# Optimization experiments

Measured on AMD Instinct MI355X. Metric: run time of the kernel, lower is better.

## Reference

```python
import jax, jax.numpy as jnp
import numpy as np

B, P, D, K = 16384, 20, 128, 5  # batch, nodes per sample, embed dim, knn k


def setup_inputs() -> dict:
    key = jax.random.key(0)
    ks = jax.random.split(key, 11)
    def rn(k, shape, scale=0.05):
        return jax.random.normal(k, shape, dtype=jnp.float32) * scale
    return {
        "x": jax.random.normal(ks[0], (B, P, D), dtype=jnp.float32),
        "W1": rn(ks[1], (300, D)), "b1": rn(ks[2], (300,)),
        "W2": rn(ks[3], (100, 300)), "b2": rn(ks[4], (100,)),
        "W3": rn(ks[5], (50, 100)), "b3": rn(ks[6], (50,)),
        "W4": rn(ks[7], (100, P * 50)), "b4": rn(ks[8], (100,)),
        "W5": rn(ks[9], (3, 100)), "b5": rn(ks[10], (3,)),
    }


def _gcn_agg_matrix(x, k):
    """Build the 20x20 GCN aggregation matrix equivalent to PyG GCNConv over the
    concatenated per-sample kNN edge lists (node ids shared 0..P-1 across batch)."""
    b, p, d = x.shape
    sq = jnp.sum(x * x, axis=-1)                                  # (B,P)
    d2 = sq[:, :, None] + sq[:, None, :] - 2.0 * jnp.einsum('bpd,bqd->bpq', x, x)
    d2 = jax.lax.stop_gradient(d2)  # indices only; squared dist preserves ordering
    _, idx = jax.lax.top_k(-d2, k + 1)                            # smallest k+1, sorted
    nbr = idx[..., 1:]                                            # (B,P,k) drop self
    src = jnp.broadcast_to(jnp.arange(p)[None, :, None], nbr.shape)
    flat = (nbr * p + src).reshape(-1)                            # C[v,u] multiplicity
    C = jnp.zeros((p * p,), jnp.float32).at[flat].add(1.0).reshape(p, p)
    deg = C.sum(axis=1) + 1.0                                     # in-degree + self-loop
    dinv = 1.0 / jnp.sqrt(deg)
    return dinv[:, None] * C * dinv[None, :] + jnp.diag(dinv * dinv)


def reference(x, W1, b1, W2, b2, W3, b3, W4, b4, W5, b5):
    h = x
    for W, b in ((W1, b1), (W2, b2), (W3, b3)):
        M = _gcn_agg_matrix(h, K)                                 # (P,P)
        h = jax.nn.relu(jnp.einsum('vu,bud->bvd', M, h @ W.T) + b)
    h = h.reshape(h.shape[0], -1)                                 # (B, P*50)
    h = jax.nn.relu(h @ W4.T + b4)
    logits = h @ W5.T + b5
    return jax.nn.softmax(logits, axis=1)
```

## Files before the change

kernel.cpp:

```cpp
#include <hip/hip_runtime.h>
#include <math.h>

#define BB 16384
#define P 20
#define NT 512

typedef short v8s __attribute__((ext_vector_type(8)));
typedef _Float16 v8h __attribute__((ext_vector_type(8)));
typedef float f32x4 __attribute__((ext_vector_type(4)));
typedef float f32x16 __attribute__((ext_vector_type(16)));

#define NELEM ((size_t)BB * P * 320)
__device__ unsigned int g_C[3][P * P];
__device__ __align__(16) unsigned short g_bufA[NELEM + 4096];
__device__ __align__(16) unsigned short g_bufB[NELEM + 4096];
__device__ __align__(16) unsigned short g_W1b[320 * 128];
__device__ __align__(16) unsigned short g_W2b[128 * 320];
__device__ __align__(16) unsigned short g_W3b[64 * 128];
__device__ __align__(16) unsigned short g_W4b[112 * 1024];
__device__ __align__(16) float g_b1p[320];
__device__ __align__(16) float g_b2p[128];
__device__ __align__(16) float g_b3p[64];
__device__ __align__(16) float g_b4p[112];

__device__ inline float bf2f(unsigned short u) {
    union { unsigned int i; float f; } c; c.i = ((unsigned int)u) << 16; return c.f;
}
__device__ inline unsigned short f2bf(float f) {
    union { float f; unsigned int i; } c; c.f = f;
    unsigned int u = c.i + 0x7fffu + ((c.i >> 16) & 1u);
    return (unsigned short)(u >> 16);
}

__global__ void zero_C_kernel() { g_C[blockIdx.x][threadIdx.x] = 0u; }

__global__ void prep_kernel(const float* __restrict__ W1, const float* __restrict__ b1,
                            const float* __restrict__ W2, const float* __restrict__ b2,
                            const float* __restrict__ W3, const float* __restrict__ b3,
                            const float* __restrict__ W4, const float* __restrict__ b4) {
    const int stride = gridDim.x * blockDim.x;
    const int id = blockIdx.x * blockDim.x + threadIdx.x;
    for (int i = id; i < 320 * 128; i += stride) { int n = i >> 7, k = i & 127;
        g_W1b[i] = (n < 300) ? f2bf(W1[n * 128 + k]) : 0; }
    for (int i = id; i < 128 * 320; i += stride) { int n = i / 320, k = i - n * 320;
        g_W2b[i] = (n < 100 && k < 300) ? f2bf(W2[n * 300 + k]) : 0; }
    for (int i = id; i < 64 * 128; i += stride) { int n = i >> 7, k = i & 127;
        g_W3b[i] = (n < 50 && k < 100) ? f2bf(W3[n * 100 + k]) : 0; }
    for (int i = id; i < 112 * 1024; i += stride) { int n = i >> 10, k = i & 1023;
        g_W4b[i] = (n < 100 && k < 1000) ? f2bf(W4[n * 1000 + k]) : 0; }
    for (int i = id; i < 320; i += stride) g_b1p[i] = (i < 300) ? b1[i] : 0.f;
    for (int i = id; i < 128; i += stride) g_b2p[i] = (i < 100) ? b2[i] : 0.f;
    for (int i = id; i < 64;  i += stride) g_b3p[i] = (i < 50)  ? b3[i] : 0.f;
    for (int i = id; i < 112; i += stride) g_b4p[i] = (i < 100) ? b4[i] : 0.f;
}

__global__ __launch_bounds__(NT)
void knn1_mfma_kernel(const float* __restrict__ x) {
    __shared__ float Gs[8][P * 21];
    __shared__ unsigned int hist[P * P];
    const int t = threadIdx.x, w = t >> 6, lane = t & 63;
    const int m31 = lane & 31, half = lane >> 5;
    const int mrow = (m31 < P) ? m31 : (P - 1);
    for (int i = t; i < P * P; i += NT) hist[i] = 0;
    for (int pass = 0; pass < 2; ++pass) {
        const size_t s = (size_t)blockIdx.x * 16 + pass * 8 + w;
        const float* rp = x + s * (size_t)(P * 128) + (size_t)mrow * 128 + half * 8;
        f32x16 acc;
#pragma unroll
        for (int i = 0; i < 16; ++i) acc[i] = 0.f;
#pragma unroll
        for (int ks = 0; ks < 8; ++ks) {
            float4 f0 = *(const float4*)(rp + ks * 16);
            float4 f1 = *(const float4*)(rp + ks * 16 + 4);
            float fv[8] = {f0.x, f0.y, f0.z, f0.w, f1.x, f1.y, f1.z, f1.w};
            v8h hi, lo;
#pragma unroll
            for (int j = 0; j < 8; ++j) {
                _Float16 hv = (_Float16)fv[j];
                hi[j] = hv;
                lo[j] = (_Float16)(fv[j] - (float)hv);
            }
            acc = __builtin_amdgcn_mfma_f32_32x32x16_f16(hi, hi, acc, 0, 0, 0);
            acc = __builtin_amdgcn_mfma_f32_32x32x16_f16(hi, lo, acc, 0, 0, 0);
            acc = __builtin_amdgcn_mfma_f32_32x32x16_f16(lo, hi, acc, 0, 0, 0);
            acc = __builtin_amdgcn_mfma_f32_32x32x16_f16(lo, lo, acc, 0, 0, 0);
        }
        float* G = &Gs[w][0];
        if (m31 < P) {
#pragma unroll
            for (int r = 0; r < 16; ++r) {
                int row = (r & 3) + 8 * (r >> 2) + 4 * half;
                if (row < P) G[row * 21 + m31] = acc[r];
            }
        }
        __syncthreads();
        if (lane < P) {
            const int p = lane;
            float d2[P];
            const float gpp = G[p * 21 + p];
#pragma unroll
            for (int u = 0; u < P; ++u)
                d2[u] = (u == p) ? 0.f : gpp + G[u * 21 + u] - 2.f * G[p * 21 + u];
            float pv = -3.0e38f; int pi = -1;
            for (int it = 0; it < 6; ++it) {
                float best = 3.0e38f; int bq = 0;
#pragma unroll
                for (int u = 0; u < P; ++u) {
                    float vu = d2[u];
                    bool cand = (vu > pv) || (vu == pv && u > pi);
                    if (cand && vu < best) { best = vu; bq = u; }
                }
                if (it > 0) atomicAdd(&hist[bq * P + p], 1u);
                pv = best; pi = bq;
            }
        }
        __syncthreads();
    }
    if (t < P * P && hist[t]) atomicAdd(&g_C[0][t], hist[t]);
}

template<int D, int CIDX>
__global__ __launch_bounds__(NT)
void knn_mfma_kernel() {
    __shared__ float Gs[8][P * 21];
    __shared__ unsigned int hist[P * P];
    const int t = threadIdx.x, w = t >> 6, lane = t & 63;
    const int m31 = lane & 31, half = lane >> 5;
    for (int i = t; i < P * P; i += NT) hist[i] = 0;
    for (int pass = 0; pass < 2; ++pass) {
        const size_t s = (size_t)blockIdx.x * 16 + pass * 8 + w;
        const unsigned short* rp = g_bufB + s * (P * D) + (size_t)m31 * D + half * 8;
        f32x16 acc;
#pragma unroll
        for (int i = 0; i < 16; ++i) acc[i] = 0.f;
        for (int ks = 0; ks < D / 16; ++ks) {
            v8s z = *(const v8s*)(rp + ks * 16);
            acc = __builtin_amdgcn_mfma_f32_32x32x16_bf16(z, z, acc, 0, 0, 0);
        }
        float* G = &Gs[w][0];
        if (m31 < P) {
#pragma unroll
            for (int r = 0; r < 16; ++r) {
                int row = (r & 3) + 8 * (r >> 2) + 4 * half;
                if (row < P) G[row * 21 + m31] = acc[r];
            }
        }
        __syncthreads();
        if (lane < P) {
            const int p = lane;
            float d2[P];
            const float gpp = G[p * 21 + p];
#pragma unroll
            for (int u = 0; u < P; ++u)
                d2[u] = (u == p) ? 0.f : gpp + G[u * 21 + u] - 2.f * G[p * 21 + u];
            float pv = -3.0e38f; int pi = -1;
            for (int it = 0; it < 6; ++it) {
                float best = 3.0e38f; int bq = 0;
#pragma unroll
                for (int u = 0; u < P; ++u) {
                    float vu = d2[u];
                    bool cand = (vu > pv) || (vu == pv && u > pi);
                    if (cand && vu < best) { best = vu; bq = u; }
                }
                if (it > 0) atomicAdd(&hist[bq * P + p], 1u);
                pv = best; pi = bq;
            }
        }
        __syncthreads();
    }
    if (t < P * P && hist[t]) atomicAdd(&g_C[CIDX][t], hist[t]);
}

__device__ inline void compute_M_512(const unsigned int* __restrict__ Cg,
                                     float* Ms, float* dinv, int t) {
    for (int i = t; i < P * P; i += 512) Ms[i] = (float)Cg[i];
    __syncthreads();
    if (t < P) {
        float deg = 1.f;
        for (int u = 0; u < P; ++u) deg += Ms[t * P + u];
        dinv[t] = 1.f / sqrtf(deg);
    }
    __syncthreads();
    for (int i = t; i < P * P; i += 512) {
        int v = i / P, u = i - v * P;
        float m = dinv[v] * Ms[i] * dinv[u];
        if (v == u) m += dinv[v] * dinv[v];
        Ms[i] = m;
    }
    __syncthreads();
}

template<int D, int CIDX>
__global__ __launch_bounds__(512)
void agg_mfma_kernel(const float* __restrict__ xin) {
    constexpr int NCB = D / 32;
    __shared__ float Ms[P * P];
    __shared__ float dinv[P];
    const int t = threadIdx.x, w = t >> 6, lane = t & 63;
    const int n31 = lane & 31, half = lane >> 5;
    compute_M_512(g_C[CIDX], Ms, dinv, t);
    v8s mhi[2], mlo[2];
#pragma unroll
    for (int kc = 0; kc < 2; ++kc)
#pragma unroll
        for (int j = 0; j < 8; ++j) {
            const int u = kc * 16 + half * 8 + j;
            const int v = n31;
            const float m = (v < P && u < P) ? Ms[v * P + u] : 0.f;
            const unsigned short h16 = f2bf(m);
            mhi[kc][j] = (short)h16;
            mlo[kc][j] = (short)f2bf(m - bf2f(h16));
        }
    const size_t s = (size_t)blockIdx.x * 8 + w;
    unsigned short* zout = g_bufA + s * (size_t)(P * D);
    const float* xr = xin + s * (size_t)(P * D);
#pragma unroll
    for (int cb = 0; cb < NCB; ++cb) {
        v8s bh0, bl0, bh1, bl1;
#pragma unroll
        for (int j = 0; j < 8; ++j) {
            const int u0 = half * 8 + j;
            int u1 = 16 + half * 8 + j; if (u1 > P - 1) u1 = P - 1;
            const float x0 = xr[(size_t)u0 * D + cb * 32 + n31];
            const float x1 = xr[(size_t)u1 * D + cb * 32 + n31];
            const unsigned short h0 = f2bf(x0), h1 = f2bf(x1);
            bh0[j] = (short)h0; bl0[j] = (short)f2bf(x0 - bf2f(h0));
            bh1[j] = (short)h1; bl1[j] = (short)f2bf(x1 - bf2f(h1));
        }
        f32x16 acc;
#pragma unroll
        for (int i = 0; i < 16; ++i) acc[i] = 0.f;
        acc = __builtin_amdgcn_mfma_f32_32x32x16_bf16(mhi[0], bh0, acc, 0, 0, 0);
        acc = __builtin_amdgcn_mfma_f32_32x32x16_bf16(mhi[0], bl0, acc, 0, 0, 0);
        acc = __builtin_amdgcn_mfma_f32_32x32x16_bf16(mlo[0], bh0, acc, 0, 0, 0);
        acc = __builtin_amdgcn_mfma_f32_32x32x16_bf16(mlo[0], bl0, acc, 0, 0, 0);
        acc = __builtin_amdgcn_mfma_f32_32x32x16_bf16(mhi[1], bh1, acc, 0, 0, 0);
        acc = __builtin_amdgcn_mfma_f32_32x32x16_bf16(mhi[1], bl1, acc, 0, 0, 0);
        acc = __builtin_amdgcn_mfma_f32_32x32x16_bf16(mlo[1], bh1, acc, 0, 0, 0);
        acc = __builtin_amdgcn_mfma_f32_32x32x16_bf16(mlo[1], bl1, acc, 0, 0, 0);
#pragma unroll
        for (int r = 0; r < 16; ++r) {
            const int row = (r & 3) + 8 * (r >> 2) + 4 * half;
            if (row < P)
                zout[(size_t)row * D + cb * 32 + n31] = f2bf(acc[r]);
        }
    }
}

template<int D, int CIDX, bool FLATOUT>
__global__ __launch_bounds__(512)
void agg_out_kernel() {
    constexpr int NCB = D / 32;
    __shared__ float Ms[P * P];
    __shared__ float dinv[P];
    const int t = threadIdx.x, w = t >> 6, lane = t & 63;
    const int n31 = lane & 31, half = lane >> 5;
    const float* __restrict__ bp = (CIDX == 1) ? g_b2p : g_b3p;
    compute_M_512(g_C[CIDX], Ms, dinv, t);
    v8s mhi[2], mlo[2];
#pragma unroll
    for (int kc = 0; kc < 2; ++kc)
#pragma unroll
        for (int j = 0; j < 8; ++j) {
            const int u = kc * 16 + half * 8 + j;
            const int v = n31;
            const float m = (v < P && u < P) ? Ms[v * P + u] : 0.f;
            const unsigned short h16 = f2bf(m);
            mhi[kc][j] = (short)h16;
            mlo[kc][j] = (short)f2bf(m - bf2f(h16));
        }
    const size_t s = (size_t)blockIdx.x * 8 + w;
    const unsigned short* yr = g_bufA + s * (size_t)(P * D);
#pragma unroll
    for (int cb = 0; cb < NCB; ++cb) {
        v8s b0, b1;
#pragma unroll
        for (int j = 0; j < 8; ++j) {
            const int u0 = half * 8 + j;
            int u1 = 16 + half * 8 + j; if (u1 > P - 1) u1 = P - 1;
            b0[j] = (short)yr[(size_t)u0 * D + cb * 32 + n31];
            b1[j] = (short)yr[(size_t)u1 * D + cb * 32 + n31];
        }
        f32x16 acc;
#pragma unroll
        for (int i = 0; i < 16; ++i) acc[i] = 0.f;
        acc = __builtin_amdgcn_mfma_f32_32x32x16_bf16(mhi[0], b0, acc, 0, 0, 0);
        acc = __builtin_amdgcn_mfma_f32_32x32x16_bf16(mlo[0], b0, acc, 0, 0, 0);
        acc = __builtin_amdgcn_mfma_f32_32x32x16_bf16(mhi[1], b1, acc, 0, 0, 0);
        acc = __builtin_amdgcn_mfma_f32_32x32x16_bf16(mlo[1], b1, acc, 0, 0, 0);
        const float bv = bp[cb * 32 + n31];
#pragma unroll
        for (int r = 0; r < 16; ++r) {
            const int row = (r & 3) + 8 * (r >> 2) + 4 * half;
            if (row < P) {
                const float val = fmaxf(acc[r] + bv, 0.f);
                if (FLATOUT) {
                    const int d = cb * 32 + n31;
                    if (d < 50)
                        g_bufB[s * 1024 + (size_t)row * 50 + d] = f2bf(val);
                } else {
                    g_bufB[(s * (size_t)P + row) * D + cb * 32 + n31] = f2bf(val);
                }
            }
        }
    }
}

__global__ __launch_bounds__(256)
void gemm2_kernel() {
    constexpr int KL = 72;
    __shared__ __align__(16) unsigned short As[128 * KL];
    __shared__ __align__(16) unsigned short Wsh[128 * KL];
    const int t = threadIdx.x, w = t >> 6, lane = t & 63;
    const int m15 = lane & 15, q = lane >> 4;
    const long row0 = (long)blockIdx.x * 128;
    f32x4 acc[2][8];
#pragma unroll
    for (int zr = 0; zr < 2; ++zr)
#pragma unroll
        for (int nf = 0; nf < 8; ++nf) acc[zr][nf] = 0.f;
    for (int kc = 0; kc < 5; ++kc) {
        __syncthreads();
        for (int i = t; i < 1024; i += 256) {
            const int r = i >> 3, c8 = i & 7;
            *(v8s*)&As[r * KL + c8 * 8] =
                *(const v8s*)(g_bufB + (size_t)(row0 + r) * 320 + kc * 64 + c8 * 8);
            *(v8s*)&Wsh[r * KL + c8 * 8] =
                *(const v8s*)(g_W2b + (size_t)r * 320 + kc * 64 + c8 * 8);
        }
        __syncthreads();
#pragma unroll
        for (int ks = 0; ks < 2; ++ks) {
            v8s af[2];
#pragma unroll
            for (int zr = 0; zr < 2; ++zr)
                af[zr] = *(const v8s*)&As[(w * 32 + zr * 16 + m15) * KL + ks * 32 + q * 8];
#pragma unroll
            for (int nf = 0; nf < 8; ++nf) {
                v8s wf = *(const v8s*)&Wsh[(nf * 16 + m15) * KL + ks * 32 + q * 8];
#pragma unroll
                for (int zr = 0; zr < 2; ++zr)
                    acc[zr][nf] = __builtin_amdgcn_mfma_f32_16x16x32_bf16(
                        wf, af[zr], acc[zr][nf], 0, 0, 0);
            }
        }
    }
#pragma unroll
    for (int zr = 0; zr < 2; ++zr) {
        const long m = row0 + w * 32 + zr * 16 + m15;
#pragma unroll
        for (int nf = 0; nf < 8; ++nf) {
            f32x4 c = acc[zr][nf];
            ushort4 o; o.x = f2bf(c[0]); o.y = f2bf(c[1]);
            o.z = f2bf(c[2]); o.w = f2bf(c[3]);
            *(ushort4*)(g_bufA + (size_t)m * 128 + nf * 16 + q * 4) = o;
        }
    }
}

template<int Kp, int Np, int ZR, bool FLAT, int WSEL, bool ATOB, int NSPLIT,
         int KSC, int NTHR, long MROWS, bool RAWBF16>
__global__ __launch_bounds__(NTHR)
void gemm_kernel() {
    constexpr int BN = Np / NSPLIT;
    constexpr int NF = BN / 16;
    constexpr int KS = Kp / 32;
    constexpr int CPT = KS / KSC;
    constexpr int KL = Kp + 8;
    constexpr int NW = NTHR / 64;
    constexpr int TM = NW * ZR * 16;
    constexpr long NTILE = MROWS / TM;
    static_assert(KS % KSC == 0, "KSC must divide KS");
    __shared__ __align__(16) unsigned short Ws[BN * KL];
    __shared__ __align__(16) float bs[BN];
    const unsigned short* __restrict__ Wb =
        (WSEL == 1) ? g_W1b : (WSEL == 2) ? g_W2b : (WSEL == 3) ? g_W3b : g_W4b;
    const float* __restrict__ bp =
        (WSEL == 1) ? g_b1p : (WSEL == 2) ? g_b2p : (WSEL == 3) ? g_b3p : g_b4p;
    const unsigned short* __restrict__ A = ATOB ? g_bufA : g_bufB;
    unsigned short* __restrict__ Hout = ATOB ? g_bufB : g_bufA;
    const int t = threadIdx.x, w = t >> 6, lane = t & 63;
    const int m15 = lane & 15, q = lane >> 4;
    const int n0 = blockIdx.y * BN;
    for (int i = t; i < BN * (Kp / 8); i += NTHR) {
        int r = i / (Kp / 8), c = i - r * (Kp / 8);
        *(v8s*)(&Ws[r * KL + c * 8]) = *(const v8s*)(Wb + (size_t)(n0 + r) * Kp + c * 8);
    }
    for (int i = t; i < BN; i += NTHR) bs[i] = bp[n0 + i];
    __syncthreads();

    v8s aC[ZR][KSC], aN[ZR][KSC];
    long tile = (long)blockIdx.x;
    if (tile < NTILE) {
        const unsigned short* ab =
            A + (size_t)(tile * TM + w * (ZR * 16) + m15) * Kp + q * 8;
#pragma unroll
        for (int zr = 0; zr < ZR; ++zr)
#pragma unroll
            for (int ks = 0; ks < KSC; ++ks)
                aC[zr][ks] = *(const v8s*)(ab + (size_t)zr * 16 * Kp + ks * 32);
    }
    for (; tile < NTILE; tile += gridDim.x) {
        f32x4 acc[ZR][NF];
#pragma unroll
        for (int zr = 0; zr < ZR; ++zr)
#pragma unroll
            for (int nf = 0; nf < NF; ++nf) acc[zr][nf] = 0.f;
        for (int c = 0; c < CPT; ++c) {
            const long ntile = (c + 1 < CPT) ? tile : tile + (long)gridDim.x;
            const int nk0 = (c + 1 < CPT) ? (c + 1) * KSC : 0;
            const bool hasNext = (ntile < NTILE);
            if (hasNext) {
                const unsigned short* ab =
                    A + (size_t)(ntile * TM + w * (ZR * 16) + m15) * Kp + nk0 * 32 + q * 8;
#pragma unroll
                for (int zr = 0; zr < ZR; ++zr)
#pragma unroll
                    for (int ks = 0; ks < KSC; ++ks)
                        aN[zr][ks] = *(const v8s*)(ab + (size_t)zr * 16 * Kp + ks * 32);
            }
#pragma unroll
            for (int nf = 0; nf < NF; ++nf) {
                v8s wr[KSC];
#pragma unroll
                for (int ks = 0; ks < KSC; ++ks)
                    wr[ks] = *(const v8s*)(&Ws[(nf * 16 + m15) * KL + (c * KSC + ks) * 32 + q * 8]);
#pragma unroll
                for (int ks = 0; ks < KSC; ++ks)
#pragma unroll
                    for (int zr = 0; zr < ZR; ++zr)
                        acc[zr][nf] = __builtin_amdgcn_mfma_f32_16x16x32_bf16(
                            wr[ks], aC[zr][ks], acc[zr][nf], 0, 0, 0);
            }
            if (hasNext) {
#pragma unroll
                for (int zr = 0; zr < ZR; ++zr)
#pragma unroll
                    for (int ks = 0; ks < KSC; ++ks) aC[zr][ks] = aN[zr][ks];
            }
        }
#pragma unroll
        for (int zr = 0; zr < ZR; ++zr) {
            const long m = tile * TM + w * (ZR * 16) + zr * 16 + m15;
#pragma unroll
            for (int nf = 0; nf < NF; ++nf) {
                f32x4 cc = acc[zr][nf];
                if (RAWBF16) {
                    ushort4 o; o.x = f2bf(cc[0]); o.y = f2bf(cc[1]);
                    o.z = f2bf(cc[2]); o.w = f2bf(cc[3]);
                    *(ushort4*)(Hout + (size_t)m * Np + n0 + nf * 16 + q * 4) = o;
                } else {
                    f32x4 b4 = *(const f32x4*)(&bs[nf * 16 + q * 4]);
                    float v0 = fmaxf(cc[0] + b4[0], 0.f), v1 = fmaxf(cc[1] + b4[1], 0.f);
                    float v2 = fmaxf(cc[2] + b4[2], 0.f), v3 = fmaxf(cc[3] + b4[3], 0.f);
                    if (!FLAT) {
                        ushort4 o; o.x = f2bf(v0); o.y = f2bf(v1); o.z = f2bf(v2); o.w = f2bf(v3);
                        *(ushort4*)(Hout + (size_t)m * Np + n0 + nf * 16 + q * 4) = o;
                    } else {
                        const int n0f = nf * 16 + q * 4;
                        if (n0f <= 48) {
                            const long s = m / 20; const int u = (int)(m - s * 20);
                            unsigned short* base = Hout + (size_t)s * 1024 + u * 50 + n0f;
                            unsigned int lo = (unsigned int)f2bf(v0) | ((unsigned int)f2bf(v1) << 16);
                            *(unsigned int*)(base) = lo;
                            if (n0f < 48) {
                                unsigned int hi = (unsigned int)f2bf(v2) | ((unsigned int)f2bf(v3) << 16);
                                *(unsigned int*)(base + 2) = hi;
                            }
                        }
                    }
                }
            }
        }
    }
}

__global__ __launch_bounds__(256)
void head_kernel(const float* __restrict__ W5, const float* __restrict__ b5,
                 float* __restrict__ out) {
    __shared__ float w5s[300];
    __shared__ float b5s[3];
    const int t = threadIdx.x;
    for (int i = t; i < 300; i += 256) w5s[i] = W5[i];
    if (t < 3) b5s[t] = b5[t];
    __syncthreads();
    const int s = blockIdx.x * 256 + t;
    const unsigned short* h = g_bufA + (size_t)s * 112;
    float a0 = b5s[0], a1 = b5s[1], a2 = b5s[2];
    for (int k = 0; k < 100; ++k) {
        float hv = bf2f(h[k]);
        a0 += hv * w5s[k]; a1 += hv * w5s[100 + k]; a2 += hv * w5s[200 + k];
    }
    float m = fmaxf(a0, fmaxf(a1, a2));
    float e0 = expf(a0 - m), e1 = expf(a1 - m), e2 = expf(a2 - m);
    float inv = 1.f / (e0 + e1 + e2);
    out[(size_t)s * 3 + 0] = e0 * inv;
    out[(size_t)s * 3 + 1] = e1 * inv;
    out[(size_t)s * 3 + 2] = e2 * inv;
}

extern "C" void kernel_launch(void* const* d_in, const int* in_sizes, int n_in,
                              void* d_out, int out_size, void* d_ws, size_t ws_size,
                              hipStream_t stream) {
    const float* x  = (const float*)d_in[0];
    const float* W1 = (const float*)d_in[1];
    const float* b1 = (const float*)d_in[2];
    const float* W2 = (const float*)d_in[3];
    const float* b2 = (const float*)d_in[4];
    const float* W3 = (const float*)d_in[5];
    const float* b3 = (const float*)d_in[6];
    const float* W4 = (const float*)d_in[7];
    const float* b4 = (const float*)d_in[8];
    const float* W5 = (const float*)d_in[9];
    const float* b5 = (const float*)d_in[10];
    float* out = (float*)d_out;

    zero_C_kernel<<<3, P * P, 0, stream>>>();
    prep_kernel<<<256, 256, 0, stream>>>(W1, b1, W2, b2, W3, b3, W4, b4);

    knn1_mfma_kernel<<<BB / 16, NT, 0, stream>>>(x);
    agg_mfma_kernel<128, 0><<<BB / 8, 512, 0, stream>>>(x);
    gemm_kernel<128, 320, 1, false, 1, true, 2, 4, 512, 327680L, false>
        <<<dim3(512, 2), 512, 0, stream>>>();

    knn_mfma_kernel<320, 1><<<BB / 16, NT, 0, stream>>>();
    gemm2_kernel<<<2560, 256, 0, stream>>>();
    agg_out_kernel<128, 1, false><<<BB / 8, 512, 0, stream>>>();

    knn_mfma_kernel<128, 2><<<BB / 16, NT, 0, stream>>>();
    gemm_kernel<128, 64, 2, false, 3, false, 1, 4, 256, 327680L, true>
        <<<dim3(512, 1), 256, 0, stream>>>();
    agg_out_kernel<64, 2, true><<<BB / 8, 512, 0, stream>>>();

    gemm_kernel<1024, 112, 1, false, 4, false, 7, 8, 256, 16384L, false>
        <<<dim3(256, 7), 256, 0, stream>>>();
    head_kernel<<<BB / 256, 256, 0, stream>>>(W5, b5, out);
}
```

Measured before the change: 808.1 us.

## Fuse layer-2 kNN graph build into the W2 GEMM kernel

```diff
diff --git a/kernel.cpp b/kernel.cpp
--- a/kernel.cpp
+++ b/kernel.cpp
@@ -32,14 +32,13 @@
     return (unsigned short)(u >> 16);
 }
 
-__global__ void zero_C_kernel() { g_C[blockIdx.x][threadIdx.x] = 0u; }
-
 __global__ void prep_kernel(const float* __restrict__ W1, const float* __restrict__ b1,
                             const float* __restrict__ W2, const float* __restrict__ b2,
                             const float* __restrict__ W3, const float* __restrict__ b3,
                             const float* __restrict__ W4, const float* __restrict__ b4) {
     const int stride = gridDim.x * blockDim.x;
     const int id = blockIdx.x * blockDim.x + threadIdx.x;
+    for (int i = id; i < 3 * P * P; i += stride) g_C[i / (P * P)][i % (P * P)] = 0u;
     for (int i = id; i < 320 * 128; i += stride) { int n = i >> 7, k = i & 127;
         g_W1b[i] = (n < 300) ? f2bf(W1[n * 128 + k]) : 0; }
     for (int i = id; i < 128 * 320; i += stride) { int n = i / 320, k = i - n * 320;
@@ -306,55 +305,93 @@
     }
 }
 
-__global__ __launch_bounds__(256)
-void gemm2_kernel() {
-    constexpr int KL = 72;
-    __shared__ __align__(16) unsigned short As[128 * KL];
-    __shared__ __align__(16) unsigned short Wsh[128 * KL];
+__global__ __launch_bounds__(640)
+void gemm2_knn_kernel() {
+    __shared__ __align__(16) unsigned short As[160 * 72];
+    __shared__ __align__(16) unsigned short Wsh[128 * 72];
+    __shared__ float Gs[8][P * 21];
+    __shared__ unsigned int hist[P * P];
     const int t = threadIdx.x, w = t >> 6, lane = t & 63;
+    const int m31 = lane & 31, half = lane >> 5;
     const int m15 = lane & 15, q = lane >> 4;
-    const long row0 = (long)blockIdx.x * 128;
-    f32x4 acc[2][8];
-#pragma unroll
-    for (int zr = 0; zr < 2; ++zr)
-#pragma unroll
-        for (int nf = 0; nf < 8; ++nf) acc[zr][nf] = 0.f;
+    const long row0 = (long)blockIdx.x * 160;
+    for (int i = t; i < P * P; i += 640) hist[i] = 0;
+    __syncthreads();
+    if (w < 8) {
+        const size_t s = (size_t)blockIdx.x * 8 + w;
+        const unsigned short* rp = g_bufB + s * (P * 320) + (size_t)m31 * 320 + half * 8;
+        f32x16 acc;
+#pragma unroll
+        for (int i = 0; i < 16; ++i) acc[i] = 0.f;
+        for (int ks = 0; ks < 20; ++ks) {
+            v8s z = *(const v8s*)(rp + ks * 16);
+            acc = __builtin_amdgcn_mfma_f32_32x32x16_bf16(z, z, acc, 0, 0, 0);
+        }
+        float* G = &Gs[w][0];
+        if (m31 < P) {
+#pragma unroll
+            for (int r = 0; r < 16; ++r) {
+                int row = (r & 3) + 8 * (r >> 2) + 4 * half;
+                if (row < P) G[row * 21 + m31] = acc[r];
+            }
+        }
+        if (lane < P) {
+            const int p = lane;
+            float d2[P];
+            const float gpp = G[p * 21 + p];
+#pragma unroll
+            for (int u = 0; u < P; ++u)
+                d2[u] = (u == p) ? 0.f : gpp + G[u * 21 + u] - 2.f * G[p * 21 + u];
+            float pv = -3.0e38f; int pi = -1;
+            for (int it = 0; it < 6; ++it) {
+                float best = 3.0e38f; int bq = 0;
+#pragma unroll
+                for (int u = 0; u < P; ++u) {
+                    float vu = d2[u];
+                    bool cand = (vu > pv) || (vu == pv && u > pi);
+                    if (cand && vu < best) { best = vu; bq = u; }
+                }
+                if (it > 0) atomicAdd(&hist[bq * P + p], 1u);
+                pv = best; pi = bq;
+            }
+        }
+    }
+    __syncthreads();
+    if (t < P * P && hist[t]) atomicAdd(&g_C[1][t], hist[t]);
+    f32x4 acc[8];
+#pragma unroll
+    for (int nf = 0; nf < 8; ++nf) acc[nf] = 0.f;
     for (int kc = 0; kc < 5; ++kc) {
         __syncthreads();
-        for (int i = t; i < 1024; i += 256) {
+        for (int i = t; i < 1280; i += 640) {
             const int r = i >> 3, c8 = i & 7;
-            *(v8s*)&As[r * KL + c8 * 8] =
+            *(v8s*)&As[r * 72 + c8 * 8] =
                 *(const v8s*)(g_bufB + (size_t)(row0 + r) * 320 + kc * 64 + c8 * 8);
-            *(v8s*)&Wsh[r * KL + c8 * 8] =
+        }
+        for (int i = t; i < 1024; i += 640) {
+            const int r = i >> 3, c8 = i & 7;
+            *(v8s*)&Wsh[r * 72 + c8 * 8] =
                 *(const v8s*)(g_W2b + (size_t)r * 320 + kc * 64 + c8 * 8);
         }
         __syncthreads();
 #pragma unroll
         for (int ks = 0; ks < 2; ++ks) {
-            v8s af[2];
-#pragma unroll
-            for (int zr = 0; zr < 2; ++zr)
-                af[zr] = *(const v8s*)&As[(w * 32 + zr * 16 + m15) * KL + ks * 32 + q * 8];
+            v8s af = *(const v8s*)&As[(w * 16 + m15) * 72 + ks * 32 + q * 8];
 #pragma unroll
             for (int nf = 0; nf < 8; ++nf) {
-                v8s wf = *(const v8s*)&Wsh[(nf * 16 + m15) * KL + ks * 32 + q * 8];
-#pragma unroll
-                for (int zr = 0; zr < 2; ++zr)
-                    acc[zr][nf] = __builtin_amdgcn_mfma_f32_16x16x32_bf16(
-                        wf, af[zr], acc[zr][nf], 0, 0, 0);
-            }
-        }
-    }
-#pragma unroll
-    for (int zr = 0; zr < 2; ++zr) {
-        const long m = row0 + w * 32 + zr * 16 + m15;
-#pragma unroll
-        for (int nf = 0; nf < 8; ++nf) {
-            f32x4 c = acc[zr][nf];
-            ushort4 o; o.x = f2bf(c[0]); o.y = f2bf(c[1]);
-            o.z = f2bf(c[2]); o.w = f2bf(c[3]);
-            *(ushort4*)(g_bufA + (size_t)m * 128 + nf * 16 + q * 4) = o;
-        }
+                v8s wf = *(const v8s*)&Wsh[(nf * 16 + m15) * 72 + ks * 32 + q * 8];
+                acc[nf] = __builtin_amdgcn_mfma_f32_16x16x32_bf16(
+                    wf, af, acc[nf], 0, 0, 0);
+            }
+        }
+    }
+    const long m = row0 + w * 16 + m15;
+#pragma unroll
+    for (int nf = 0; nf < 8; ++nf) {
+        f32x4 c = acc[nf];
+        ushort4 o; o.x = f2bf(c[0]); o.y = f2bf(c[1]);
+        o.z = f2bf(c[2]); o.w = f2bf(c[3]);
+        *(ushort4*)(g_bufA + (size_t)m * 128 + nf * 16 + q * 4) = o;
     }
 }
 
@@ -515,7 +552,6 @@
     const float* b5 = (const float*)d_in[10];
     float* out = (float*)d_out;
 
-    zero_C_kernel<<<3, P * P, 0, stream>>>();
     prep_kernel<<<256, 256, 0, stream>>>(W1, b1, W2, b2, W3, b3, W4, b4);
 
     knn1_mfma_kernel<<<BB / 16, NT, 0, stream>>>(x);
@@ -523,8 +559,7 @@
     gemm_kernel<128, 320, 1, false, 1, true, 2, 4, 512, 327680L, false>
         <<<dim3(512, 2), 512, 0, stream>>>();
 
-    knn_mfma_kernel<320, 1><<<BB / 16, NT, 0, stream>>>();
-    gemm2_kernel<<<2560, 256, 0, stream>>>();
+    gemm2_knn_kernel<<<BB / 8, 640, 0, stream>>>();
     agg_out_kernel<128, 1, false><<<BB / 8, 512, 0, stream>>>();
 
     knn_mfma_kernel<128, 2><<<BB / 16, NT, 0, stream>>>();
```

After: 871.7 us. +7.9%, slower.
